# Performance work log

Measured on AMD Instinct MI355X. Metric: run time of the kernel, lower is better.

## Reference

```python
import jax, jax.numpy as jnp
import numpy as np

B, S, D, H, R = 2, 2048, 1024, 16, 64
DD = D // H  # head depth = 64
EPS = 1e-06


def setup_inputs() -> dict:
    key = jax.random.key(0)
    ks = jax.random.split(key, 12)
    sc = 1.0 / np.sqrt(D)
    inp = {
        'v': jax.random.normal(ks[0], (B, S, D), jnp.float32),
        'k': jax.random.normal(ks[1], (B, S, D), jnp.float32),
        'q': jax.random.normal(ks[2], (B, S, D), jnp.float32),
        'wq_w': jax.random.normal(ks[3], (D, D), jnp.float32) * sc,
        'wq_b': jnp.zeros((D,), jnp.float32),
        'wk_w': jax.random.normal(ks[4], (D, D), jnp.float32) * sc,
        'wk_b': jnp.zeros((D,), jnp.float32),
        'wv_w': jax.random.normal(ks[5], (D, D), jnp.float32) * sc,
        'wv_b': jnp.zeros((D,), jnp.float32),
        'wc_w': jax.random.normal(ks[6], (D, D), jnp.float32) * sc,
        'wc_b': jnp.zeros((D,), jnp.float32),
        # random-feature projection (orthogonal in original; gaussian suffices for a math-equivalent reference)
        'wg': jax.random.normal(ks[7], (H, DD, R), jnp.float32) * (1.0 / np.sqrt(DD)),
    }
    return inp


def _split_heads(x):
    # [B,S,D] -> [B,H,S,DD]
    return x.reshape(B, S, H, DD).transpose(0, 2, 1, 3)


def _combine_heads(x):
    # [B,H,S,DD] -> [B,S,D]
    return x.transpose(0, 2, 1, 3).reshape(B, S, D)


def _sm_approx(x, wg):
    # x: [B,H,S,DD], wg: [H,DD,R] -> phi(x): [B,H,S,R]
    rsqr_d = 1.0 / np.sqrt(DD)
    h_x = jnp.exp(-0.5 * jnp.sum(jnp.square(x), axis=-1, keepdims=True))
    phi_x = rsqr_d * jnp.exp(jnp.einsum('bhsd,hdr->bhsr', x, wg))
    return h_x * phi_x


def reference(v, k, q, wq_w, wq_b, wk_w, wk_b, wv_w, wv_b, wc_w, wc_b, wg):
    norm_d = float(DD) ** -0.25
    qh = _split_heads((q @ wq_w + wq_b) * norm_d)   # [B,H,S,DD]
    kh = _split_heads((k @ wk_w + wk_b) * norm_d)   # [B,H,S,DD]
    vh = _split_heads(v @ wv_w + wv_b)              # [B,H,S,DD]

    q_prime = _sm_approx(qh, wg)                    # [B,H,S,R]
    k_prime = _sm_approx(kh, wg)                    # [B,H,S,R]

    # per-position outer product k_prime (x) v : [B,H,S,R,DD]
    kv_prime = jnp.einsum('bhsr,bhsd->bhsrd', k_prime, vh)

    # causal prefix sums over sequence axis (k_prev/kv_prev = 0 case)
    k_prefix = jnp.cumsum(k_prime, axis=2)          # [B,H,S,R]
    kv_prefix = jnp.cumsum(kv_prime, axis=2)        # [B,H,S,R,DD]

    qk_prefix = jnp.sum(q_prime * k_prefix, axis=-1, keepdims=True)       # [B,H,S,1]
    attn_unnorm = jnp.einsum('bhsr,bhsrd->bhsd', q_prime, kv_prefix)      # [B,H,S,DD]
    attn = attn_unnorm / (EPS + qk_prefix)

    out = _combine_heads(attn) @ wc_w + wc_b        # [B,S,D]
    return (k_prefix, kv_prefix, out)
```

## Files before the change

### kernel.cpp

```cpp
#include <hip/hip_runtime.h>
#include <hip/hip_bf16.h>

#define BB 2
#define SS 2048
#define DD 1024
#define HH 16
#define RR 64
#define DH 64
#define BH (BB*HH)
#define MM (BB*SS)
#define CH 32
#define NCH (SS/CH)
#define CSROW (RR*DH + RR)

using short8 = __attribute__((ext_vector_type(8))) short;
using f32x4  = __attribute__((ext_vector_type(4))) float;

__global__ __launch_bounds__(256) void k_prep(
    const float* __restrict__ q, const float* __restrict__ k, const float* __restrict__ v,
    const float* __restrict__ bq, const float* __restrict__ bk, const float* __restrict__ bv,
    __hip_bfloat16* __restrict__ Xb, float* __restrict__ biasb)
{
    int z = blockIdx.y;
    const float* src = (z == 0) ? q : (z == 1) ? k : v;
    size_t i = ((size_t)blockIdx.x * 256 + threadIdx.x) * 4;
    float4 f = *(const float4*)(src + i);
    __hip_bfloat16* dst = Xb + (size_t)z * 4194304 + i;
    dst[0] = __float2bfloat16(f.x);
    dst[1] = __float2bfloat16(f.y);
    dst[2] = __float2bfloat16(f.z);
    dst[3] = __float2bfloat16(f.w);
    if (blockIdx.x == 0 && threadIdx.x < 1024) {
        const float* bb = (z == 0) ? bq : (z == 1) ? bk : bv;
        biasb[z * 1024 + threadIdx.x] = bb[threadIdx.x];
    }
}

__global__ __launch_bounds__(256) void k_wt(
    const float* __restrict__ wq, const float* __restrict__ wk,
    const float* __restrict__ wv, const float* __restrict__ wc,
    __hip_bfloat16* __restrict__ WT, __hip_bfloat16* __restrict__ wcT)
{
    int z = blockIdx.z;
    const float* W = (z == 0) ? wq : (z == 1) ? wk : (z == 2) ? wv : wc;
    __hip_bfloat16* T = (z < 3) ? (WT + (size_t)z * 1048576) : wcT;
    __shared__ float tile[64][65];
    int k0 = blockIdx.y * 64, n0 = blockIdx.x * 64;
    for (int i = threadIdx.x; i < 4096; i += 256) {
        int r = i >> 6, cc = i & 63;
        tile[r][cc] = W[(size_t)(k0 + r) * 1024 + n0 + cc];
    }
    __syncthreads();
    for (int i = threadIdx.x; i < 4096; i += 256) {
        int nl = i >> 6, kl = i & 63;
        T[(size_t)(n0 + nl) * 1024 + k0 + kl] = __float2bfloat16(tile[kl][nl]);
    }
}

__global__ __launch_bounds__(256) void gemm_bt(
    const __hip_bfloat16* __restrict__ X, const __hip_bfloat16* __restrict__ WT,
    const float* __restrict__ bias, float* __restrict__ Cout,
    long zsX, long zsW, long zsB, long zsC, int applyNorm)
{
    const int K = 1024, N = 1024;
    int z = blockIdx.z;
    const short* Xz = (const short*)(X + (size_t)z * zsX);
    const short* Wz = (const short*)(WT + (size_t)z * zsW);
    const float* bz = bias + (size_t)z * zsB;
    float* Cz = Cout + (size_t)z * zsC;
    float scale = (applyNorm && z < 2) ? 0.35355339059327373f : 1.0f;

    __shared__ short As[128 * 32];
    __shared__ short Bs[128 * 32];
    int tid = threadIdx.x;
    int m0 = blockIdx.y * 128;
    int n0 = blockIdx.x * 128;
    int lane = tid & 63;
    int w = tid >> 6;
    int wm = (w >> 1) * 64, wn = (w & 1) * 64;

    f32x4 acc[4][4] = {};

    int srow = tid >> 2;
    int scol = (tid & 3) * 8;
    const short* Ag = Xz + (size_t)(m0 + srow) * K + scol;
    const short* Bg = Wz + (size_t)(n0 + srow) * K + scol;

    int fr = lane & 15, kg = (lane >> 4) * 8;

    for (int kt = 0; kt < K / 32; ++kt) {
        short8 a0 = *(const short8*)(Ag + kt * 32);
        short8 a1 = *(const short8*)(Ag + (size_t)64 * K + kt * 32);
        short8 b0 = *(const short8*)(Bg + kt * 32);
        short8 b1 = *(const short8*)(Bg + (size_t)64 * K + kt * 32);
        __syncthreads();
        *(short8*)&As[srow * 32 + scol] = a0;
        *(short8*)&As[(64 + srow) * 32 + scol] = a1;
        *(short8*)&Bs[srow * 32 + scol] = b0;
        *(short8*)&Bs[(64 + srow) * 32 + scol] = b1;
        __syncthreads();

        short8 af[4], bf[4];
#pragma unroll
        for (int mi = 0; mi < 4; ++mi)
            af[mi] = *(const short8*)&As[(wm + mi * 16 + fr) * 32 + kg];
#pragma unroll
        for (int ni = 0; ni < 4; ++ni)
            bf[ni] = *(const short8*)&Bs[(wn + ni * 16 + fr) * 32 + kg];
#pragma unroll
        for (int mi = 0; mi < 4; ++mi)
#pragma unroll
            for (int ni = 0; ni < 4; ++ni)
                acc[mi][ni] = __builtin_amdgcn_mfma_f32_16x16x32_bf16(af[mi], bf[ni], acc[mi][ni], 0, 0, 0);
    }

    int rg = (lane >> 4) * 4;
#pragma unroll
    for (int mi = 0; mi < 4; ++mi)
#pragma unroll
        for (int ni = 0; ni < 4; ++ni) {
            int gn = n0 + wn + ni * 16 + fr;
            float bval = bz[gn];
#pragma unroll
            for (int i = 0; i < 4; ++i) {
                int gm = m0 + wm + mi * 16 + rg + i;
                Cz[(size_t)gm * N + gn] = (acc[mi][ni][i] + bval) * scale;
            }
        }
}

__global__ __launch_bounds__(256) void k_phi(
    const float* __restrict__ qh, const float* __restrict__ kh,
    const float* __restrict__ wg,
    float* __restrict__ qprime, float* __restrict__ kprime)
{
    int z = blockIdx.z;
    int bh = blockIdx.y;
    int b = bh >> 4, h = bh & 15;
    int s0 = blockIdx.x * 64;
    int tid = threadIdx.x, lane = tid & 63, w = tid >> 6;
    const float* X = (z == 0) ? qh : kh;
    float* O = (z == 0) ? qprime : kprime;

    float wgc[DH];
#pragma unroll
    for (int dd = 0; dd < DH; ++dd)
        wgc[dd] = wg[((size_t)h * DH + dd) * RR + lane];

    __shared__ float xs[64][DH];
    for (int i = tid; i < 64 * DH; i += 256) {
        int rr = i >> 6, dd = i & 63;
        xs[rr][dd] = X[((size_t)b * SS + s0 + rr) * DD + h * DH + dd];
    }
    __syncthreads();

    for (int rr = w; rr < 64; rr += 4) {
        float arg = 0.f, nrm = 0.f;
#pragma unroll
        for (int d4 = 0; d4 < 16; ++d4) {
            float4 xq = *(const float4*)&xs[rr][d4 * 4];
            arg += xq.x * wgc[d4 * 4 + 0] + xq.y * wgc[d4 * 4 + 1]
                 + xq.z * wgc[d4 * 4 + 2] + xq.w * wgc[d4 * 4 + 3];
            nrm += xq.x * xq.x + xq.y * xq.y + xq.z * xq.z + xq.w * xq.w;
        }
        O[((size_t)bh * SS + s0 + rr) * RR + lane] = 0.125f * __expf(arg - 0.5f * nrm);
    }
}

__global__ __launch_bounds__(64) void k_chunksum(
    const float* __restrict__ kprime, const float* __restrict__ vh,
    float* __restrict__ cs)
{
    int c = blockIdx.x;
    int bh = blockIdx.y;
    int b = bh >> 4, h = bh & 15;
    int lane = threadIdx.x;
    __shared__ float kp[CH][RR];
    size_t rowbase = (size_t)bh * SS + c * CH;
    for (int i = 0; i < CH; ++i)
        kp[i][lane] = kprime[(rowbase + i) * RR + lane];
    __syncthreads();

    float st[RR];
#pragma unroll
    for (int r = 0; r < RR; ++r) st[r] = 0.f;
    float kpsum = 0.f;
    const float* vptr = vh + ((size_t)b * SS + c * CH) * DD + h * DH + lane;
    for (int s = 0; s < CH; ++s) {
        float vd = vptr[(size_t)s * DD];
        kpsum += kp[s][lane];
#pragma unroll
        for (int rq = 0; rq < RR / 4; ++rq) {
            float4 kq = *(const float4*)&kp[s][rq * 4];
            st[rq * 4 + 0] += kq.x * vd;
            st[rq * 4 + 1] += kq.y * vd;
            st[rq * 4 + 2] += kq.z * vd;
            st[rq * 4 + 3] += kq.w * vd;
        }
    }
    float* out = cs + (size_t)(bh * NCH + c) * CSROW;
#pragma unroll
    for (int r = 0; r < RR; ++r) out[r * 64 + lane] = st[r];
    out[4096 + lane] = kpsum;
}

__global__ __launch_bounds__(256) void k_scan(float* __restrict__ cs)
{
    int t = blockIdx.x * 256 + threadIdx.x;
    if (t >= BH * CSROW) return;
    int bh = t / CSROW;
    int e = t - bh * CSROW;
    float run = 0.f;
    float* p = cs + (size_t)bh * NCH * CSROW + e;
    for (int c = 0; c < NCH; ++c) {
        float v = p[(size_t)c * CSROW];
        p[(size_t)c * CSROW] = run;
        run += v;
    }
}

__global__ __launch_bounds__(64) void k_scanfinal(
    const float* __restrict__ kprime, const float* __restrict__ qprime,
    const float* __restrict__ vh, const float* __restrict__ cs,
    float* __restrict__ kp_out, float* __restrict__ kv_out,
    __hip_bfloat16* __restrict__ attnb)
{
    int c = blockIdx.x;
    int bh = blockIdx.y;
    int b = bh >> 4, h = bh & 15;
    int lane = threadIdx.x;
    __shared__ float kp[CH][RR];
    __shared__ float qp[CH][RR];
    size_t rowbase = (size_t)bh * SS + c * CH;
    for (int i = 0; i < CH; ++i) {
        kp[i][lane] = kprime[(rowbase + i) * RR + lane];
        qp[i][lane] = qprime[(rowbase + i) * RR + lane];
    }
    __syncthreads();

    const float* off = cs + (size_t)(bh * NCH + c) * CSROW;
    float st[RR];
#pragma unroll
    for (int r = 0; r < RR; ++r) st[r] = off[r * 64 + lane];
    float kps = off[4096 + lane];

    const float* vptr = vh + ((size_t)b * SS + c * CH) * DD + h * DH + lane;
    for (int s = 0; s < CH; ++s) {
        float vd = vptr[(size_t)s * DD];
        kps += kp[s][lane];
        size_t srow = rowbase + s;
        kp_out[srow * RR + lane] = kps;

        float qksum = qp[s][lane] * kps;
#pragma unroll
        for (int m = 1; m < 64; m <<= 1) qksum += __shfl_xor(qksum, m, 64);

        float accd = 0.f;
        float* kvp = kv_out + srow * (size_t)(RR * DH) + lane;
#pragma unroll
        for (int rq = 0; rq < RR / 4; ++rq) {
            float4 kq = *(const float4*)&kp[s][rq * 4];
            float4 qq = *(const float4*)&qp[s][rq * 4];
            st[rq * 4 + 0] += kq.x * vd; accd += qq.x * st[rq * 4 + 0];
            __builtin_nontemporal_store(st[rq * 4 + 0], kvp + (rq * 4 + 0) * 64);
            st[rq * 4 + 1] += kq.y * vd; accd += qq.y * st[rq * 4 + 1];
            __builtin_nontemporal_store(st[rq * 4 + 1], kvp + (rq * 4 + 1) * 64);
            st[rq * 4 + 2] += kq.z * vd; accd += qq.z * st[rq * 4 + 2];
            __builtin_nontemporal_store(st[rq * 4 + 2], kvp + (rq * 4 + 2) * 64);
            st[rq * 4 + 3] += kq.w * vd; accd += qq.w * st[rq * 4 + 3];
            __builtin_nontemporal_store(st[rq * 4 + 3], kvp + (rq * 4 + 3) * 64);
        }
        float attn = accd / (1e-6f + qksum);
        int s_abs = c * CH + s;
        attnb[((size_t)b * SS + s_abs) * DD + h * DH + lane] = __float2bfloat16(attn);
    }
}

extern "C" void kernel_launch(void* const* d_in, const int* in_sizes, int n_in,
                              void* d_out, int out_size, void* d_ws, size_t ws_size,
                              hipStream_t stream) {
    const float* v_in  = (const float*)d_in[0];
    const float* k_in  = (const float*)d_in[1];
    const float* q_in  = (const float*)d_in[2];
    const float* wq_w  = (const float*)d_in[3];
    const float* wq_b  = (const float*)d_in[4];
    const float* wk_w  = (const float*)d_in[5];
    const float* wk_b  = (const float*)d_in[6];
    const float* wv_w  = (const float*)d_in[7];
    const float* wv_b  = (const float*)d_in[8];
    const float* wc_w  = (const float*)d_in[9];
    const float* wc_b  = (const float*)d_in[10];
    const float* wg    = (const float*)d_in[11];

    char* ws = (char*)d_ws;
    __hip_bfloat16* Xb    = (__hip_bfloat16*)(ws + 0);
    __hip_bfloat16* WT    = (__hip_bfloat16*)(ws + 25165824);
    __hip_bfloat16* wcT   = (__hip_bfloat16*)(ws + 31457280);
    float* biasb          = (float*)(ws + 33554432);
    float* qhkv           = (float*)(ws + 33570816);
    float* qprime         = (float*)(ws + 83902464);
    float* kprime         = (float*)(ws + 100679680);
    float* cs             = (float*)(ws + 117456896);
    __hip_bfloat16* attnb = (__hip_bfloat16*)(ws + 151535616);

    float* kp_out = (float*)d_out;
    float* kv_out = kp_out + 4194304;
    float* out_o  = kv_out + 268435456;

    k_prep<<<dim3(4096, 3), 256, 0, stream>>>(q_in, k_in, v_in, wq_b, wk_b, wv_b, Xb, biasb);
    k_wt<<<dim3(16, 16, 4), 256, 0, stream>>>(wq_w, wk_w, wv_w, wc_w, WT, wcT);
    gemm_bt<<<dim3(8, 32, 3), 256, 0, stream>>>(Xb, WT, biasb, qhkv,
                                                4194304L, 1048576L, 1024L, 4194304L, 1);
    k_phi<<<dim3(32, 32, 2), 256, 0, stream>>>(qhkv, qhkv + 4194304, wg, qprime, kprime);
    k_chunksum<<<dim3(NCH, BH), 64, 0, stream>>>(kprime, qhkv + 2 * 4194304, cs);
    k_scan<<<dim3(520), 256, 0, stream>>>(cs);
    k_scanfinal<<<dim3(NCH, BH), 64, 0, stream>>>(kprime, qprime, qhkv + 2 * 4194304, cs,
                                                  kp_out, kv_out, attnb);
    gemm_bt<<<dim3(8, 32, 1), 256, 0, stream>>>(attnb, wcT, wc_b, out_o, 0L, 0L, 0L, 0L, 0);
}
```

Before: 391.4 us.

## Merge prep kernels, use direct global-to-LDS loads in GEMM, batch scan loads

Fuses the input-conversion and weight-transpose kernels into one launch, so one kernel launch and one inter-kernel gap go away. The GEMM now stages tiles with global_load_lds (16 bytes per lane) straight into shared memory instead of going through registers, which is meant to free VGPRs and cut issue overhead. The chunk scan loads all 64 chunk values before the serial prefix loop so the loads can overlap. Risks: the fused launch spawns many blocks that exit immediately, and the global_load_lds lane-to-LDS layout must match the tile layout.

```diff
diff --git a/kernel.cpp b/kernel.cpp
--- a/kernel.cpp
+++ b/kernel.cpp
@@ -16,44 +16,51 @@
 using short8 = __attribute__((ext_vector_type(8))) short;
 using f32x4  = __attribute__((ext_vector_type(4))) float;
 
-__global__ __launch_bounds__(256) void k_prep(
+typedef const __attribute__((address_space(1))) unsigned int* gp_t;
+typedef __attribute__((address_space(3))) unsigned int* lp_t;
+
+__device__ __forceinline__ void gll16(const void* g, void* l) {
+    __builtin_amdgcn_global_load_lds((gp_t)g, (lp_t)l, 16, 0, 0);
+}
+
+__global__ __launch_bounds__(256) void k_pre(
     const float* __restrict__ q, const float* __restrict__ k, const float* __restrict__ v,
     const float* __restrict__ bq, const float* __restrict__ bk, const float* __restrict__ bv,
-    __hip_bfloat16* __restrict__ Xb, float* __restrict__ biasb)
-{
-    int z = blockIdx.y;
-    const float* src = (z == 0) ? q : (z == 1) ? k : v;
-    size_t i = ((size_t)blockIdx.x * 256 + threadIdx.x) * 4;
-    float4 f = *(const float4*)(src + i);
-    __hip_bfloat16* dst = Xb + (size_t)z * 4194304 + i;
-    dst[0] = __float2bfloat16(f.x);
-    dst[1] = __float2bfloat16(f.y);
-    dst[2] = __float2bfloat16(f.z);
-    dst[3] = __float2bfloat16(f.w);
-    if (blockIdx.x == 0 && threadIdx.x < 1024) {
-        const float* bb = (z == 0) ? bq : (z == 1) ? bk : bv;
-        biasb[z * 1024 + threadIdx.x] = bb[threadIdx.x];
-    }
-}
-
-__global__ __launch_bounds__(256) void k_wt(
     const float* __restrict__ wq, const float* __restrict__ wk,
     const float* __restrict__ wv, const float* __restrict__ wc,
+    __hip_bfloat16* __restrict__ Xb, float* __restrict__ biasb,
     __hip_bfloat16* __restrict__ WT, __hip_bfloat16* __restrict__ wcT)
 {
-    int z = blockIdx.z;
-    const float* W = (z == 0) ? wq : (z == 1) ? wk : (z == 2) ? wv : wc;
-    __hip_bfloat16* T = (z < 3) ? (WT + (size_t)z * 1048576) : wcT;
+    int z = blockIdx.y;
     __shared__ float tile[64][65];
-    int k0 = blockIdx.y * 64, n0 = blockIdx.x * 64;
-    for (int i = threadIdx.x; i < 4096; i += 256) {
-        int r = i >> 6, cc = i & 63;
-        tile[r][cc] = W[(size_t)(k0 + r) * 1024 + n0 + cc];
-    }
-    __syncthreads();
-    for (int i = threadIdx.x; i < 4096; i += 256) {
-        int nl = i >> 6, kl = i & 63;
-        T[(size_t)(n0 + nl) * 1024 + k0 + kl] = __float2bfloat16(tile[kl][nl]);
+    if (z < 3) {
+        const float* src = (z == 0) ? q : (z == 1) ? k : v;
+        size_t i = ((size_t)blockIdx.x * 256 + threadIdx.x) * 4;
+        float4 f = *(const float4*)(src + i);
+        __hip_bfloat16* dst = Xb + (size_t)z * 4194304 + i;
+        dst[0] = __float2bfloat16(f.x);
+        dst[1] = __float2bfloat16(f.y);
+        dst[2] = __float2bfloat16(f.z);
+        dst[3] = __float2bfloat16(f.w);
+        if (blockIdx.x == 0 && threadIdx.x < 1024) {
+            const float* bb = (z == 0) ? bq : (z == 1) ? bk : bv;
+            biasb[z * 1024 + threadIdx.x] = bb[threadIdx.x];
+        }
+    } else {
+        if (blockIdx.x >= 256) return;
+        int zz = z - 3;
+        const float* W = (zz == 0) ? wq : (zz == 1) ? wk : (zz == 2) ? wv : wc;
+        __hip_bfloat16* T = (zz < 3) ? (WT + (size_t)zz * 1048576) : wcT;
+        int k0 = (blockIdx.x >> 4) * 64, n0 = (blockIdx.x & 15) * 64;
+        for (int i = threadIdx.x; i < 4096; i += 256) {
+            int r = i >> 6, cc = i & 63;
+            tile[r][cc] = W[(size_t)(k0 + r) * 1024 + n0 + cc];
+        }
+        __syncthreads();
+        for (int i = threadIdx.x; i < 4096; i += 256) {
+            int nl = i >> 6, kl = i & 63;
+            T[(size_t)(n0 + nl) * 1024 + k0 + kl] = __float2bfloat16(tile[kl][nl]);
+        }
     }
 }
 
@@ -85,19 +92,19 @@
     int scol = (tid & 3) * 8;
     const short* Ag = Xz + (size_t)(m0 + srow) * K + scol;
     const short* Bg = Wz + (size_t)(n0 + srow) * K + scol;
+    short* lA0 = As + tid * 8;
+    short* lA1 = As + 64 * 32 + tid * 8;
+    short* lB0 = Bs + tid * 8;
+    short* lB1 = Bs + 64 * 32 + tid * 8;
 
     int fr = lane & 15, kg = (lane >> 4) * 8;
 
     for (int kt = 0; kt < K / 32; ++kt) {
-        short8 a0 = *(const short8*)(Ag + kt * 32);
-        short8 a1 = *(const short8*)(Ag + (size_t)64 * K + kt * 32);
-        short8 b0 = *(const short8*)(Bg + kt * 32);
-        short8 b1 = *(const short8*)(Bg + (size_t)64 * K + kt * 32);
         __syncthreads();
-        *(short8*)&As[srow * 32 + scol] = a0;
-        *(short8*)&As[(64 + srow) * 32 + scol] = a1;
-        *(short8*)&Bs[srow * 32 + scol] = b0;
-        *(short8*)&Bs[(64 + srow) * 32 + scol] = b1;
+        gll16(Ag + kt * 32, lA0);
+        gll16(Ag + (size_t)64 * K + kt * 32, lA1);
+        gll16(Bg + kt * 32, lB0);
+        gll16(Bg + (size_t)64 * K + kt * 32, lB1);
         __syncthreads();
 
         short8 af[4], bf[4];
@@ -210,12 +217,16 @@
     if (t >= BH * CSROW) return;
     int bh = t / CSROW;
     int e = t - bh * CSROW;
+    float* p = cs + (size_t)bh * NCH * CSROW + e;
+    float v[NCH];
+#pragma unroll
+    for (int c = 0; c < NCH; ++c) v[c] = p[(size_t)c * CSROW];
     float run = 0.f;
-    float* p = cs + (size_t)bh * NCH * CSROW + e;
+#pragma unroll
     for (int c = 0; c < NCH; ++c) {
-        float v = p[(size_t)c * CSROW];
+        float x = v[c];
         p[(size_t)c * CSROW] = run;
-        run += v;
+        run += x;
     }
 }
 
@@ -307,8 +318,8 @@
     float* kv_out = kp_out + 4194304;
     float* out_o  = kv_out + 268435456;
 
-    k_prep<<<dim3(4096, 3), 256, 0, stream>>>(q_in, k_in, v_in, wq_b, wk_b, wv_b, Xb, biasb);
-    k_wt<<<dim3(16, 16, 4), 256, 0, stream>>>(wq_w, wk_w, wv_w, wc_w, WT, wcT);
+    k_pre<<<dim3(4096, 7), 256, 0, stream>>>(q_in, k_in, v_in, wq_b, wk_b, wv_b,
+                                             wq_w, wk_w, wv_w, wc_w, Xb, biasb, WT, wcT);
     gemm_bt<<<dim3(8, 32, 3), 256, 0, stream>>>(Xb, WT, biasb, qhkv,
                                                 4194304L, 1048576L, 1024L, 4194304L, 1);
     k_phi<<<dim3(32, 32, 2), 256, 0, stream>>>(qhkv, qhkv + 4194304, wg, qprime, kprime);
```

New measurement: 393.5 us. Within noise of the previous version (+0.5%).
